# Kernel optimization log

Measured on AMD Instinct MI355X. Metric: run time of the kernel, lower is better.

The kernel has to match this reference:

```python
import jax, jax.numpy as jnp
import numpy as np

N, E = 50000, 800000
F_IN, EDGE_DIM, H, C = 128, 64, 8, 32
NEG_SLOPE = 0.2


def setup_inputs() -> dict:
    key = jax.random.key(0)
    ks = jax.random.split(key, 9)
    return {
        "x": jax.random.normal(ks[0], (N, F_IN), dtype=jnp.float32),
        "edge_index": jax.random.randint(ks[1], (2, E), 0, N, dtype=jnp.int32),
        "edge_attr": jax.random.normal(ks[2], (E, EDGE_DIM), dtype=jnp.float32),
        "W": jax.random.normal(ks[3], (F_IN, H * C), dtype=jnp.float32) * 0.05,
        "att_src": jax.random.normal(ks[4], (H, C), dtype=jnp.float32) * 0.05,
        "att_dst": jax.random.normal(ks[5], (H, C), dtype=jnp.float32) * 0.05,
        "W_edge": jax.random.normal(ks[6], (EDGE_DIM, H * C), dtype=jnp.float32) * 0.05,
        "att_edge": jax.random.normal(ks[7], (H, C), dtype=jnp.float32) * 0.05,
        "bias": jax.random.normal(ks[8], (H * C,), dtype=jnp.float32) * 0.05,
    }


def reference(x, edge_index, edge_attr, W, att_src, att_dst, W_edge, att_edge, bias):
    src, dst = edge_index[0], edge_index[1]  # messages flow src -> dst
    # Pre-activation ReLU from Graph_intra.forward
    xr = jax.nn.relu(x)
    # Linear projection, per-head view: [N, H, C]
    xs = (xr @ W).reshape(N, H, C)
    # Per-node attention logits: [N, H]
    a_src = jnp.einsum("nhc,hc->nh", xs, att_src)
    a_dst = jnp.einsum("nhc,hc->nh", xs, att_dst)
    # Edge-feature attention contribution: [E, H]
    e_proj = (edge_attr @ W_edge).reshape(E, H, C)
    a_edge = jnp.einsum("ehc,hc->eh", e_proj, att_edge)
    # Per-edge logits + LeakyReLU
    alpha = jax.nn.leaky_relu(a_src[src] + a_dst[dst] + a_edge, NEG_SLOPE)  # [E, H]
    # Segment softmax over destination neighborhoods
    seg_max = jax.ops.segment_max(alpha, dst, num_segments=N)
    seg_max = jnp.where(jnp.isfinite(seg_max), seg_max, 0.0)
    alpha = jnp.exp(alpha - seg_max[dst])
    seg_sum = jax.ops.segment_sum(alpha, dst, num_segments=N)
    alpha = alpha / (seg_sum[dst] + 1e-16)
    # Weighted message aggregation: scatter-add alpha_e * x_src[e]
    msgs = alpha[:, :, None] * xs[src]  # [E, H, C]
    out = jax.ops.segment_sum(msgs, dst, num_segments=N)  # [N, H, C]
    return out.reshape(N, H * C) + bias
```

## Files before the change

kernel.cpp:

```cpp
#include <hip/hip_runtime.h>

#define N_NODES 50000
#define E_EDGES 800000
#define F_IN    128
#define EDGE_DIM 64
#define HC      256
#define NEG_SLOPE 0.2f

typedef __attribute__((ext_vector_type(8))) short short8;
typedef __attribute__((ext_vector_type(4))) float f32x4;

__device__ __forceinline__ unsigned short f2bf(float f) {
    unsigned u = __builtin_bit_cast(unsigned, f);
    u += 0x7fffu + ((u >> 16) & 1u);
    return (unsigned short)(u >> 16);
}
__device__ __forceinline__ float bf2f(unsigned short b) {
    return __builtin_bit_cast(float, (unsigned)b << 16);
}

__global__ __launch_bounds__(256) void k_pre(const float* __restrict__ W,
        const float* __restrict__ att_src, const float* __restrict__ att_dst,
        const float* __restrict__ W_edge, const float* __restrict__ att_edge,
        unsigned short* __restrict__ W_T, unsigned short* __restrict__ WaT,
        unsigned short* __restrict__ WaE, int* __restrict__ counts, int* __restrict__ gcur) {
    int idx = blockIdx.x * 256 + threadIdx.x;
    if (idx < N_NODES) counts[idx] = 0;
    if (idx == 0) *gcur = 0;
    if (idx < 32768) {
        int n = idx >> 7, k = idx & 127;
        W_T[n * 128 + k] = f2bf(W[k * 256 + n]);
    }
    if (idx < 2048) {
        int col = idx & 15, k = idx >> 4;
        const float* att = (col < 8) ? att_src : att_dst;
        int h = col & 7;
        float s = 0.f;
        #pragma unroll
        for (int c = 0; c < 32; ++c)
            s = fmaf(W[k * 256 + h * 32 + c], att[h * 32 + c], s);
        WaT[col * 128 + k] = f2bf(s);
    }
    if (idx < 1024) {
        int c = idx >> 6, k = idx & 63;
        float s = 0.f;
        if (c < 8) {
            #pragma unroll
            for (int cc = 0; cc < 32; ++cc)
                s = fmaf(W_edge[k * 256 + c * 32 + cc], att_edge[c * 32 + cc], s);
        }
        WaE[c * 64 + k] = (c < 8) ? f2bf(s) : (unsigned short)0;
    }
}

#define NT_TILES 782
#define K1_GRID 512
#define HIST_BLOCKS 782
__global__ __launch_bounds__(256, 2) void k1h(const float* __restrict__ x,
        const unsigned short* __restrict__ W_T, const unsigned short* __restrict__ WaT,
        const int4* __restrict__ dst4, int* __restrict__ counts, int4* __restrict__ slot4,
        unsigned short* __restrict__ xs, float* __restrict__ a_src, float* __restrict__ a_dst) {
    __shared__ unsigned short sB[256 * 128];
    __shared__ unsigned short sA[64 * 128];
    int t = threadIdx.x;

    if (blockIdx.x < HIST_BLOCKS) {
        int i = blockIdx.x * 256 + t;
        if (i < E_EDGES / 4) {
            int4 d = dst4[i];
            int4 sl;
            sl.x = atomicAdd(&counts[d.x], 1);
            sl.y = atomicAdd(&counts[d.y], 1);
            sl.z = atomicAdd(&counts[d.z], 1);
            sl.w = atomicAdd(&counts[d.w], 1);
            slot4[i] = sl;
        }
        return;
    }
    int bid = blockIdx.x - HIST_BLOCKS;

    for (int G = t; G < 4096; G += 256) {
        int n = G >> 4, gi = G & 15;
        *(int4*)&sB[(n * 16 + (gi ^ (n & 7))) * 8] = *(const int4*)&W_T[n * 128 + gi * 8];
    }
    int lane = t & 63, w = t >> 6, mr = lane & 15, g = lane >> 4;
    short8 wa[4];
    #pragma unroll
    for (int ks = 0; ks < 4; ++ks)
        wa[ks] = *(const short8*)&WaT[mr * 128 + ks * 32 + g * 8];

    bool first = true;
    for (int rt = bid; rt < NT_TILES; rt += K1_GRID) {
        if (!first) __syncthreads();
        first = false;
        for (int G = t; G < 1024; G += 256) {
            int r = G >> 4, gi = G & 15;
            int node = rt * 64 + r;
            unsigned short pk[8];
            if (node < N_NODES) {
                const float* xp = &x[(long)node * 128 + gi * 8];
                #pragma unroll
                for (int jj = 0; jj < 8; ++jj) pk[jj] = f2bf(fmaxf(xp[jj], 0.f));
            } else {
                #pragma unroll
                for (int jj = 0; jj < 8; ++jj) pk[jj] = 0;
            }
            *(int4*)&sA[(r * 16 + (gi ^ (r & 7))) * 8] = *(int4*)pk;
        }
        __syncthreads();

        f32x4 acc[17];
        #pragma unroll
        for (int i = 0; i < 17; ++i) acc[i] = (f32x4){0.f, 0.f, 0.f, 0.f};

        int r16 = w * 16 + mr;
        #pragma unroll
        for (int ks = 0; ks < 4; ++ks) {
            int pos = (ks * 4 + g) ^ (mr & 7);
            short8 a = *(const short8*)&sA[(r16 * 16 + pos) * 8];
            #pragma unroll
            for (int nt = 0; nt < 16; ++nt) {
                short8 b = *(const short8*)&sB[((nt * 16 + mr) * 16 + pos) * 8];
                acc[nt] = __builtin_amdgcn_mfma_f32_16x16x32_bf16(a, b, acc[nt], 0, 0, 0);
            }
            acc[16] = __builtin_amdgcn_mfma_f32_16x16x32_bf16(a, wa[ks], acc[16], 0, 0, 0);
        }

        #pragma unroll
        for (int r = 0; r < 4; ++r) {
            int node = rt * 64 + w * 16 + g * 4 + r;
            if (node < N_NODES) {
                #pragma unroll
                for (int nt = 0; nt < 16; ++nt)
                    xs[(long)node * 256 + nt * 16 + mr] = f2bf(acc[nt][r]);
                if (mr < 8) a_src[node * 8 + mr]       = acc[16][r];
                else        a_dst[node * 8 + (mr - 8)] = acc[16][r];
            }
        }
    }
}

__global__ __launch_bounds__(256) void k4_alloc(const int* __restrict__ counts,
                                                int* __restrict__ starts,
                                                int* __restrict__ gcur) {
    int n = blockIdx.x * 256 + threadIdx.x;
    int c = (n < N_NODES) ? counts[n] : 0;
    int incl = c;
    #pragma unroll
    for (int off = 1; off < 64; off <<= 1) {
        int u = __shfl_up(incl, off);
        if ((threadIdx.x & 63) >= off) incl += u;
    }
    int total = __shfl(incl, 63);
    int wavebase = 0;
    if ((threadIdx.x & 63) == 63) wavebase = atomicAdd(gcur, total);
    wavebase = __shfl(wavebase, 63);
    if (n < N_NODES) starts[n] = wavebase + incl - c;
}

__global__ __launch_bounds__(256) void k25_mfma(const float* __restrict__ ea,
        const unsigned short* __restrict__ WaE,
        const int* __restrict__ src, const int* __restrict__ dst,
        const int* __restrict__ slot, const int* __restrict__ starts,
        const float* __restrict__ a_src, const float* __restrict__ a_dst,
        _Float16* __restrict__ w_perm, int* __restrict__ src_perm) {
    __shared__ int s_sn[256], s_dn[256], s_pos[256];
    int t = threadIdx.x;
    int blockbase = blockIdx.x * 256;
    {
        int e = blockbase + t;
        int dn = dst[e], sn = src[e];
        int pos = starts[dn] + slot[e];
        s_sn[t] = sn; s_dn[t] = dn; s_pos[t] = pos;
        src_perm[pos] = sn;
    }
    __syncthreads();
    int lane = t & 63, w = t >> 6;
    int mr = lane & 15, g = lane >> 4;
    short8 b0 = *(const short8*)&WaE[mr * 64 + g * 8];
    short8 b1 = *(const short8*)&WaE[mr * 64 + 32 + g * 8];

    #pragma unroll
    for (int ti = 0; ti < 4; ++ti) {
        int lb = w * 64 + ti * 16;
        int er = blockbase + lb + mr;
        const float* ap = &ea[(size_t)er * 64 + g * 8];
        short8 a0, a1;
        #pragma unroll
        for (int j = 0; j < 8; ++j) a0[j] = (short)f2bf(ap[j]);
        #pragma unroll
        for (int j = 0; j < 8; ++j) a1[j] = (short)f2bf(ap[32 + j]);
        f32x4 acc = (f32x4){0.f, 0.f, 0.f, 0.f};
        acc = __builtin_amdgcn_mfma_f32_16x16x32_bf16(a0, b0, acc, 0, 0, 0);
        acc = __builtin_amdgcn_mfma_f32_16x16x32_bf16(a1, b1, acc, 0, 0, 0);
        if (mr < 8) {
            #pragma unroll
            for (int r = 0; r < 4; ++r) {
                int le = lb + g * 4 + r;
                int sn = s_sn[le], dn = s_dn[le];
                float v = acc[r] + a_src[sn * 8 + mr] + a_dst[dn * 8 + mr];
                v = (v > 0.f) ? v : NEG_SLOPE * v;
                w_perm[(size_t)s_pos[le] * 8 + mr] = (_Float16)__expf(v);
            }
        }
    }
}

__global__ __launch_bounds__(256) void k6_wave(
    const int* __restrict__ starts, const int* __restrict__ counts,
    const _Float16* __restrict__ w_perm, const int* __restrict__ src_perm,
    const unsigned short* __restrict__ xs, const float* __restrict__ bias,
    float* __restrict__ out) {
    int lane = threadIdx.x & 63;
    int n = blockIdx.x * 4 + (threadIdx.x >> 6);
    if (n >= N_NODES) return;
    int start = starts[n], cnt = counts[n];
    int j = lane >> 3;
    int hq = lane >> 3;

    float acc0 = 0.f, acc1 = 0.f, acc2 = 0.f, acc3 = 0.f;
    float psum = 0.f;
    for (int base = 0; base < cnt; base += 8) {
        int nk = cnt - base; if (nk > 8) nk = 8;
        float wv = (float)w_perm[(size_t)(start + base) * 8 + lane];
        if (j >= nk) wv = 0.f;
        psum += wv;
        int sv = src_perm[start + base + (lane & 7)];
        #pragma unroll
        for (int jj = 0; jj < 8; ++jj) {
            int s = __shfl(sv, jj);
            s = (jj < nk) ? s : 0;
            float w = __shfl(wv, jj * 8 + hq);
            ushort4 xv = *(const ushort4*)&xs[(size_t)s * 256 + lane * 4];
            acc0 = fmaf(w, bf2f(xv.x), acc0);
            acc1 = fmaf(w, bf2f(xv.y), acc1);
            acc2 = fmaf(w, bf2f(xv.z), acc2);
            acc3 = fmaf(w, bf2f(xv.w), acc3);
        }
    }
    psum += __shfl_xor(psum, 8);
    psum += __shfl_xor(psum, 16);
    psum += __shfl_xor(psum, 32);
    float denom = __shfl(psum, hq);
    float rinv = 1.0f / (denom + 1e-16f);
    float4 bv = *(const float4*)&bias[lane * 4];
    f32x4 o;
    o[0] = acc0 * rinv + bv.x;
    o[1] = acc1 * rinv + bv.y;
    o[2] = acc2 * rinv + bv.z;
    o[3] = acc3 * rinv + bv.w;
    __builtin_nontemporal_store(o, (f32x4*)&out[(size_t)n * 256 + lane * 4]);
}

extern "C" void kernel_launch(void* const* d_in, const int* in_sizes, int n_in,
                              void* d_out, int out_size, void* d_ws, size_t ws_size,
                              hipStream_t stream) {
    const float* x         = (const float*)d_in[0];
    const int*   ei        = (const int*)d_in[1];
    const float* edge_attr = (const float*)d_in[2];
    const float* W         = (const float*)d_in[3];
    const float* att_src   = (const float*)d_in[4];
    const float* att_dst   = (const float*)d_in[5];
    const float* W_edge    = (const float*)d_in[6];
    const float* att_edge  = (const float*)d_in[7];
    const float* bias      = (const float*)d_in[8];
    float* out = (float*)d_out;

    const int* e_src = ei;
    const int* e_dst = ei + E_EDGES;

    char* p = (char*)d_ws;
    unsigned short* xs = (unsigned short*)p; p += (size_t)N_NODES * HC * 2;
    float* a_src   = (float*)p; p += (size_t)N_NODES * 8 * 4;
    float* a_dst   = (float*)p; p += (size_t)N_NODES * 8 * 4;
    _Float16* w_perm = (_Float16*)p; p += (size_t)E_EDGES * 8 * 2 + 256;
    int* src_perm  = (int*)p;   p += (size_t)E_EDGES * 4 + 256;
    int* slot      = (int*)p;   p += (size_t)E_EDGES * 4 + 256;
    unsigned short* W_T  = (unsigned short*)p; p += 32768 * 2;
    unsigned short* WaT  = (unsigned short*)p; p += 2048 * 2;
    unsigned short* WaE  = (unsigned short*)p; p += 1024 * 2;
    int* counts    = (int*)p;   p += 200192;
    int* starts    = (int*)p;   p += 200192;
    int* gcur      = (int*)p;   p += 256;

    hipLaunchKernelGGL(k_pre, dim3(196), dim3(256), 0, stream,
                       W, att_src, att_dst, W_edge, att_edge, W_T, WaT, WaE, counts, gcur);
    hipLaunchKernelGGL(k1h, dim3(HIST_BLOCKS + K1_GRID), dim3(256), 0, stream,
                       x, W_T, WaT, (const int4*)e_dst, counts, (int4*)slot, xs, a_src, a_dst);
    hipLaunchKernelGGL(k4_alloc, dim3(196), dim3(256), 0, stream,
                       counts, starts, gcur);
    hipLaunchKernelGGL(k25_mfma, dim3(E_EDGES / 256), dim3(256), 0, stream,
                       edge_attr, WaE, e_src, e_dst, slot, starts,
                       a_src, a_dst, w_perm, src_perm);
    hipLaunchKernelGGL(k6_wave, dim3(N_NODES / 4), dim3(256), 0, stream,
                       starts, counts, w_perm, src_perm, xs, bias, out);
}
```

Baseline: 209.3 us.

## Split attention logits from projection GEMM and overlap GEMM with edge-logit kernel

The per-node attention logits (a_src/a_dst) move into a small MFMA kernel that runs alongside the histogram. The full xs projection GEMM is then fused into one launch with the edge-logit/permutation work, so the two independent phases can run concurrently on the GPU. The aim is to take the xs GEMM off the critical path before the scan and hide it behind the edge-bound work. In exchange, x is read twice, and the GEMM blocks' 80KB shared-memory request now also applies to the edge blocks, which limits how many of them fit on a CU at once.

```diff
diff --git a/kernel.cpp b/kernel.cpp
--- a/kernel.cpp
+++ b/kernel.cpp
@@ -53,17 +53,13 @@
     }
 }
 
-#define NT_TILES 782
-#define K1_GRID 512
 #define HIST_BLOCKS 782
-__global__ __launch_bounds__(256, 2) void k1h(const float* __restrict__ x,
-        const unsigned short* __restrict__ W_T, const unsigned short* __restrict__ WaT,
+#define ALOG_BLOCKS 782
+__global__ __launch_bounds__(256) void kA(const float* __restrict__ x,
+        const unsigned short* __restrict__ WaT,
         const int4* __restrict__ dst4, int* __restrict__ counts, int4* __restrict__ slot4,
-        unsigned short* __restrict__ xs, float* __restrict__ a_src, float* __restrict__ a_dst) {
-    __shared__ unsigned short sB[256 * 128];
-    __shared__ unsigned short sA[64 * 128];
+        float* __restrict__ a_src, float* __restrict__ a_dst) {
     int t = threadIdx.x;
-
     if (blockIdx.x < HIST_BLOCKS) {
         int i = blockIdx.x * 256 + t;
         if (i < E_EDGES / 4) {
@@ -77,20 +73,113 @@
         }
         return;
     }
-    int bid = blockIdx.x - HIST_BLOCKS;
-
+    int tile = (blockIdx.x - HIST_BLOCKS) * 4 + (t >> 6);
+    if (tile >= N_NODES / 16) return;
+    int lane = t & 63, mr = lane & 15, g = lane >> 4;
+    int node = tile * 16 + mr;
+    f32x4 acc = (f32x4){0.f, 0.f, 0.f, 0.f};
+    #pragma unroll
+    for (int ks = 0; ks < 4; ++ks) {
+        const float* xp = &x[(size_t)node * 128 + ks * 32 + g * 8];
+        short8 a;
+        #pragma unroll
+        for (int j = 0; j < 8; ++j) a[j] = (short)f2bf(fmaxf(xp[j], 0.f));
+        short8 b = *(const short8*)&WaT[mr * 128 + ks * 32 + g * 8];
+        acc = __builtin_amdgcn_mfma_f32_16x16x32_bf16(a, b, acc, 0, 0, 0);
+    }
+    #pragma unroll
+    for (int r = 0; r < 4; ++r) {
+        int n2 = tile * 16 + g * 4 + r;
+        if (mr < 8) a_src[n2 * 8 + mr]       = acc[r];
+        else        a_dst[n2 * 8 + (mr - 8)] = acc[r];
+    }
+}
+
+__global__ __launch_bounds__(256) void kB_alloc(const int* __restrict__ counts,
+                                                int* __restrict__ starts,
+                                                int* __restrict__ gcur) {
+    int n = blockIdx.x * 256 + threadIdx.x;
+    int c = (n < N_NODES) ? counts[n] : 0;
+    int incl = c;
+    #pragma unroll
+    for (int off = 1; off < 64; off <<= 1) {
+        int u = __shfl_up(incl, off);
+        if ((threadIdx.x & 63) >= off) incl += u;
+    }
+    int total = __shfl(incl, 63);
+    int wavebase = 0;
+    if ((threadIdx.x & 63) == 63) wavebase = atomicAdd(gcur, total);
+    wavebase = __shfl(wavebase, 63);
+    if (n < N_NODES) starts[n] = wavebase + incl - c;
+}
+
+#define NT_TILES 782
+#define K1_GRID 512
+__global__ __launch_bounds__(256, 2) void kC(const float* __restrict__ x,
+        const unsigned short* __restrict__ W_T, const unsigned short* __restrict__ WaE,
+        const float* __restrict__ ea,
+        const int* __restrict__ src, const int* __restrict__ dst,
+        const int* __restrict__ slot, const int* __restrict__ starts,
+        const float* __restrict__ a_src, const float* __restrict__ a_dst,
+        unsigned short* __restrict__ xs,
+        _Float16* __restrict__ w_perm, int* __restrict__ src_perm) {
+    __shared__ __align__(16) char smem[81920];
+    int t = threadIdx.x;
+
+    if (blockIdx.x >= K1_GRID) {
+        int* s_sn  = (int*)smem;
+        int* s_dn  = (int*)(smem + 1024);
+        int* s_pos = (int*)(smem + 2048);
+        int blockbase = (blockIdx.x - K1_GRID) * 256;
+        {
+            int e = blockbase + t;
+            int dn = dst[e], sn = src[e];
+            int pos = starts[dn] + slot[e];
+            s_sn[t] = sn; s_dn[t] = dn; s_pos[t] = pos;
+            src_perm[pos] = sn;
+        }
+        __syncthreads();
+        int lane = t & 63, w = t >> 6;
+        int mr = lane & 15, g = lane >> 4;
+        short8 b0 = *(const short8*)&WaE[mr * 64 + g * 8];
+        short8 b1 = *(const short8*)&WaE[mr * 64 + 32 + g * 8];
+        #pragma unroll
+        for (int ti = 0; ti < 4; ++ti) {
+            int lb = w * 64 + ti * 16;
+            int er = blockbase + lb + mr;
+            const float* ap = &ea[(size_t)er * 64 + g * 8];
+            short8 a0, a1;
+            #pragma unroll
+            for (int j = 0; j < 8; ++j) a0[j] = (short)f2bf(ap[j]);
+            #pragma unroll
+            for (int j = 0; j < 8; ++j) a1[j] = (short)f2bf(ap[32 + j]);
+            f32x4 acc = (f32x4){0.f, 0.f, 0.f, 0.f};
+            acc = __builtin_amdgcn_mfma_f32_16x16x32_bf16(a0, b0, acc, 0, 0, 0);
+            acc = __builtin_amdgcn_mfma_f32_16x16x32_bf16(a1, b1, acc, 0, 0, 0);
+            if (mr < 8) {
+                #pragma unroll
+                for (int r = 0; r < 4; ++r) {
+                    int le = lb + g * 4 + r;
+                    int sn = s_sn[le], dn = s_dn[le];
+                    float v = acc[r] + a_src[sn * 8 + mr] + a_dst[dn * 8 + mr];
+                    v = (v > 0.f) ? v : NEG_SLOPE * v;
+                    w_perm[(size_t)s_pos[le] * 8 + mr] = (_Float16)__expf(v);
+                }
+            }
+        }
+        return;
+    }
+
+    unsigned short* sB = (unsigned short*)smem;
+    unsigned short* sA = (unsigned short*)(smem + 65536);
     for (int G = t; G < 4096; G += 256) {
         int n = G >> 4, gi = G & 15;
         *(int4*)&sB[(n * 16 + (gi ^ (n & 7))) * 8] = *(const int4*)&W_T[n * 128 + gi * 8];
     }
     int lane = t & 63, w = t >> 6, mr = lane & 15, g = lane >> 4;
-    short8 wa[4];
-    #pragma unroll
-    for (int ks = 0; ks < 4; ++ks)
-        wa[ks] = *(const short8*)&WaT[mr * 128 + ks * 32 + g * 8];
 
     bool first = true;
-    for (int rt = bid; rt < NT_TILES; rt += K1_GRID) {
+    for (int rt = blockIdx.x; rt < NT_TILES; rt += K1_GRID) {
         if (!first) __syncthreads();
         first = false;
         for (int G = t; G < 1024; G += 256) {
@@ -109,9 +198,9 @@
         }
         __syncthreads();
 
-        f32x4 acc[17];
-        #pragma unroll
-        for (int i = 0; i < 17; ++i) acc[i] = (f32x4){0.f, 0.f, 0.f, 0.f};
+        f32x4 acc[16];
+        #pragma unroll
+        for (int i = 0; i < 16; ++i) acc[i] = (f32x4){0.f, 0.f, 0.f, 0.f};
 
         int r16 = w * 16 + mr;
         #pragma unroll
@@ -123,7 +212,6 @@
                 short8 b = *(const short8*)&sB[((nt * 16 + mr) * 16 + pos) * 8];
                 acc[nt] = __builtin_amdgcn_mfma_f32_16x16x32_bf16(a, b, acc[nt], 0, 0, 0);
             }
-            acc[16] = __builtin_amdgcn_mfma_f32_16x16x32_bf16(a, wa[ks], acc[16], 0, 0, 0);
         }
 
         #pragma unroll
@@ -133,74 +221,6 @@
                 #pragma unroll
                 for (int nt = 0; nt < 16; ++nt)
                     xs[(long)node * 256 + nt * 16 + mr] = f2bf(acc[nt][r]);
-                if (mr < 8) a_src[node * 8 + mr]       = acc[16][r];
-                else        a_dst[node * 8 + (mr - 8)] = acc[16][r];
-            }
-        }
-    }
-}
-
-__global__ __launch_bounds__(256) void k4_alloc(const int* __restrict__ counts,
-                                                int* __restrict__ starts,
-                                                int* __restrict__ gcur) {
-    int n = blockIdx.x * 256 + threadIdx.x;
-    int c = (n < N_NODES) ? counts[n] : 0;
-    int incl = c;
-    #pragma unroll
-    for (int off = 1; off < 64; off <<= 1) {
-        int u = __shfl_up(incl, off);
-        if ((threadIdx.x & 63) >= off) incl += u;
-    }
-    int total = __shfl(incl, 63);
-    int wavebase = 0;
-    if ((threadIdx.x & 63) == 63) wavebase = atomicAdd(gcur, total);
-    wavebase = __shfl(wavebase, 63);
-    if (n < N_NODES) starts[n] = wavebase + incl - c;
-}
-
-__global__ __launch_bounds__(256) void k25_mfma(const float* __restrict__ ea,
-        const unsigned short* __restrict__ WaE,
-        const int* __restrict__ src, const int* __restrict__ dst,
-        const int* __restrict__ slot, const int* __restrict__ starts,
-        const float* __restrict__ a_src, const float* __restrict__ a_dst,
-        _Float16* __restrict__ w_perm, int* __restrict__ src_perm) {
-    __shared__ int s_sn[256], s_dn[256], s_pos[256];
-    int t = threadIdx.x;
-    int blockbase = blockIdx.x * 256;
-    {
-        int e = blockbase + t;
-        int dn = dst[e], sn = src[e];
-        int pos = starts[dn] + slot[e];
-        s_sn[t] = sn; s_dn[t] = dn; s_pos[t] = pos;
-        src_perm[pos] = sn;
-    }
-    __syncthreads();
-    int lane = t & 63, w = t >> 6;
-    int mr = lane & 15, g = lane >> 4;
-    short8 b0 = *(const short8*)&WaE[mr * 64 + g * 8];
-    short8 b1 = *(const short8*)&WaE[mr * 64 + 32 + g * 8];
-
-    #pragma unroll
-    for (int ti = 0; ti < 4; ++ti) {
-        int lb = w * 64 + ti * 16;
-        int er = blockbase + lb + mr;
-        const float* ap = &ea[(size_t)er * 64 + g * 8];
-        short8 a0, a1;
-        #pragma unroll
-        for (int j = 0; j < 8; ++j) a0[j] = (short)f2bf(ap[j]);
-        #pragma unroll
-        for (int j = 0; j < 8; ++j) a1[j] = (short)f2bf(ap[32 + j]);
-        f32x4 acc = (f32x4){0.f, 0.f, 0.f, 0.f};
-        acc = __builtin_amdgcn_mfma_f32_16x16x32_bf16(a0, b0, acc, 0, 0, 0);
-        acc = __builtin_amdgcn_mfma_f32_16x16x32_bf16(a1, b1, acc, 0, 0, 0);
-        if (mr < 8) {
-            #pragma unroll
-            for (int r = 0; r < 4; ++r) {
-                int le = lb + g * 4 + r;
-                int sn = s_sn[le], dn = s_dn[le];
-                float v = acc[r] + a_src[sn * 8 + mr] + a_dst[dn * 8 + mr];
-                v = (v > 0.f) ? v : NEG_SLOPE * v;
-                w_perm[(size_t)s_pos[le] * 8 + mr] = (_Float16)__expf(v);
             }
         }
     }
@@ -285,13 +305,13 @@
 
     hipLaunchKernelGGL(k_pre, dim3(196), dim3(256), 0, stream,
                        W, att_src, att_dst, W_edge, att_edge, W_T, WaT, WaE, counts, gcur);
-    hipLaunchKernelGGL(k1h, dim3(HIST_BLOCKS + K1_GRID), dim3(256), 0, stream,
-                       x, W_T, WaT, (const int4*)e_dst, counts, (int4*)slot, xs, a_src, a_dst);
-    hipLaunchKernelGGL(k4_alloc, dim3(196), dim3(256), 0, stream,
+    hipLaunchKernelGGL(kA, dim3(HIST_BLOCKS + ALOG_BLOCKS), dim3(256), 0, stream,
+                       x, WaT, (const int4*)e_dst, counts, (int4*)slot, a_src, a_dst);
+    hipLaunchKernelGGL(kB_alloc, dim3(196), dim3(256), 0, stream,
                        counts, starts, gcur);
-    hipLaunchKernelGGL(k25_mfma, dim3(E_EDGES / 256), dim3(256), 0, stream,
-                       edge_attr, WaE, e_src, e_dst, slot, starts,
-                       a_src, a_dst, w_perm, src_perm);
+    hipLaunchKernelGGL(kC, dim3(K1_GRID + E_EDGES / 256), dim3(256), 0, stream,
+                       x, W_T, WaE, edge_attr, e_src, e_dst, slot, starts,
+                       a_src, a_dst, xs, w_perm, src_perm);
     hipLaunchKernelGGL(k6_wave, dim3(N_NODES / 4), dim3(256), 0, stream,
                        starts, counts, w_perm, src_perm, xs, bias, out);
 }
```

Result: no change. 211.2 us (+0.9%).
